# Kernel tuning notes

Measured on AMD Instinct MI355X. Metric: run time of the kernel, lower is better.

Reference implementation:

```python
import jax, jax.numpy as jnp
import numpy as np

N, H = 8192, 1024

def setup_inputs() -> dict:
    key = jax.random.key(0)
    ks = jax.random.split(key, 7)
    s = 1.0 / np.sqrt(H)
    return {
        "x": jax.random.normal(ks[0], (N, H), dtype=jnp.float32),
        "Wq": jax.random.uniform(ks[1], (H, H), dtype=jnp.float32, minval=-s, maxval=s),
        "bq": jax.random.uniform(ks[2], (H,), dtype=jnp.float32, minval=-s, maxval=s),
        "Wk": jax.random.uniform(ks[3], (H, H), dtype=jnp.float32, minval=-s, maxval=s),
        "bk": jax.random.uniform(ks[4], (H,), dtype=jnp.float32, minval=-s, maxval=s),
        "Wv": jax.random.uniform(ks[5], (H, H), dtype=jnp.float32, minval=-s, maxval=s),
        "bv": jax.random.uniform(ks[6], (H,), dtype=jnp.float32, minval=-s, maxval=s),
    }

def reference(x, Wq, bq, Wk, bk, Wv, bv):
    # q/k/v projections: [N, H]
    q = x @ Wq + bq
    k = x @ Wk + bk
    v = x @ Wv + bv
    # full scores [N, N]; NOTE: original has no 1/sqrt(d) scaling
    scores = q @ k.T
    alpha = jax.nn.softmax(scores, axis=1)
    return alpha @ v
```

## Files before the change

### kernel.cpp

```cpp
#include <hip/hip_runtime.h>
#include <hip/hip_bf16.h>
#include <hip/hip_fp16.h>


typedef _Float16 f16x8 __attribute__((ext_vector_type(8)));
typedef float floatx4 __attribute__((ext_vector_type(4)));

__device__ __forceinline__ unsigned short f2h(float f) {
  __half h = __float2half(f);
  return __builtin_bit_cast(unsigned short, h);
}
__device__ __forceinline__ float h2f(unsigned short u) {
  return __half2float(__builtin_bit_cast(__half, u));
}

__device__ __forceinline__ void async16(const void* g, void* l) {
  __builtin_amdgcn_global_load_lds(
      (__attribute__((address_space(1))) unsigned int*)(g),
      (__attribute__((address_space(3))) unsigned int*)(l),
      16, 0, 0);
}


__global__ __launch_bounds__(256) void conv_f32_f16(const float* __restrict__ in,
                                                    unsigned short* __restrict__ out,
                                                    long n) {
  long i = ((long)blockIdx.x * 256 + threadIdx.x) * 4;
  if (i + 3 < n) {
    float4 f = *(const float4*)(in + i);
    ushort4 o;
    o.x = f2h(f.x); o.y = f2h(f.y); o.z = f2h(f.z); o.w = f2h(f.w);
    *(ushort4*)(out + i) = o;
  }
}

__global__ __launch_bounds__(256) void transpose_f32_f16_3(const float* __restrict__ in0,
                                                           const float* __restrict__ in1,
                                                           const float* __restrict__ in2,
                                                           unsigned short* __restrict__ out,
                                                           int rows, int cols) {
  const float* in = (blockIdx.z == 0) ? in0 : (blockIdx.z == 1) ? in1 : in2;
  unsigned short* o = out + (size_t)blockIdx.z * rows * cols;
  __shared__ float tile[32][33];
  int bx = blockIdx.x * 32;
  int by = blockIdx.y * 32;
  int tx = threadIdx.x & 31, ty = threadIdx.x >> 5;
  #pragma unroll
  for (int yy = ty; yy < 32; yy += 8)
    tile[yy][tx] = in[(size_t)(by + yy) * cols + bx + tx];
  __syncthreads();
  #pragma unroll
  for (int yy = ty; yy < 32; yy += 8)
    o[(size_t)(bx + yy) * rows + by + tx] = f2h(tile[tx][yy]);
}

template <int MODE>
__global__ __launch_bounds__(256, 4)
void gemm_bt(const unsigned short* __restrict__ A,
             const unsigned short* __restrict__ B,
             int M, int Nn, int K,
             const float* __restrict__ b0, const float* __restrict__ b1,
             const float* __restrict__ b2,
             unsigned short* __restrict__ out) {
  if constexpr (MODE == 0) {
    B   += (size_t)blockIdx.z * Nn * K;
    out += (size_t)blockIdx.z * M * Nn;
  }
  const float* bias = (MODE != 0) ? nullptr
                      : (blockIdx.z == 0) ? b0 : (blockIdx.z == 1) ? b1 : b2;
  __shared__ unsigned short As[128 * 32];
  __shared__ unsigned short Bs[128 * 32];
  const int tid  = threadIdx.x;
  const int wave = tid >> 6;
  const int lane = tid & 63;
  const int wm = wave >> 1, wn = wave & 1;
  const int quad = lane >> 4, l16 = lane & 15;
  const long bm = (long)blockIdx.y * 128;
  const long bn = (long)blockIdx.x * 128;

  floatx4 acc[4][4] = {};

  const int srow = wave * 32 + (lane >> 2);
  const int scol = (lane & 3) * 8;
  const unsigned short* gA0 = A + (bm + srow) * (long)K + scol;
  const unsigned short* gA1 = gA0 + 16L * K;
  const unsigned short* gB0 = B + (bn + srow) * (long)K + scol;
  const unsigned short* gB1 = gB0 + 16L * K;
  unsigned short* lA0 = &As[(wave * 32) * 32];
  unsigned short* lA1 = &As[(wave * 32 + 16) * 32];
  unsigned short* lB0 = &Bs[(wave * 32) * 32];
  unsigned short* lB1 = &Bs[(wave * 32 + 16) * 32];

  for (int kk = 0; kk < K; kk += 32) {
    async16(gA0 + kk, lA0);
    async16(gA1 + kk, lA1);
    async16(gB0 + kk, lB0);
    async16(gB1 + kk, lB1);
    __syncthreads();
    f16x8 af[4], bfv[4];
    #pragma unroll
    for (int i = 0; i < 4; ++i) {
      af[i]  = *reinterpret_cast<const f16x8*>(&As[(wm * 64 + i * 16 + l16) * 32 + quad * 8]);
      bfv[i] = *reinterpret_cast<const f16x8*>(&Bs[(wn * 64 + i * 16 + l16) * 32 + quad * 8]);
    }
    #pragma unroll
    for (int i = 0; i < 4; ++i)
      #pragma unroll
      for (int j = 0; j < 4; ++j)
        acc[i][j] = __builtin_amdgcn_mfma_f32_16x16x32_f16(af[i], bfv[j], acc[i][j], 0, 0, 0);
    __syncthreads();
  }

  #pragma unroll
  for (int i = 0; i < 4; ++i) {
    const long row0 = bm + wm * 64 + i * 16 + quad * 4;
    #pragma unroll
    for (int j = 0; j < 4; ++j) {
      const long col = bn + wn * 64 + j * 16 + l16;
      const float cb = (MODE == 0) ? bias[col] : 0.0f;
      #pragma unroll
      for (int r = 0; r < 4; ++r)
        out[(row0 + r) * (long)Nn + col] = f2h(acc[i][j][r] + cb);
    }
  }
}

__global__ __launch_bounds__(256) void softmax_compact(unsigned short* __restrict__ S,
                                                       int* __restrict__ nnz, int n) {
  const int row = blockIdx.x;
  const int tid = threadIdx.x;
  const int lane = tid & 63, w = tid >> 6;
  unsigned short* prow = S + (size_t)row * n;
  const __half* hrow = (const __half*)prow;

  float v[32];
  float m = -1e30f;
  #pragma unroll
  for (int i = 0; i < 32; ++i) {
    v[i] = __half2float(hrow[i * 256 + tid]);
    m = fmaxf(m, v[i]);
  }
  #pragma unroll
  for (int off = 32; off > 0; off >>= 1) m = fmaxf(m, __shfl_down(m, off, 64));
  __shared__ float redm[4];
  __shared__ int cnt;
  if (lane == 0) redm[w] = m;
  if (tid == 0) cnt = 0;
  __syncthreads();
  m = fmaxf(fmaxf(redm[0], redm[1]), fmaxf(redm[2], redm[3]));

  float s = 0.0f;
  #pragma unroll
  for (int i = 0; i < 32; ++i) {
    v[i] = __expf(v[i] - m);
    s += v[i];
  }
  #pragma unroll
  for (int off = 32; off > 0; off >>= 1) s += __shfl_down(s, off, 64);
  __shared__ float reds[4];
  if (lane == 0) reds[w] = s;
  __syncthreads();
  s = reds[0] + reds[1] + reds[2] + reds[3];
  const float inv = 1.0f / s;

  unsigned int* pairs = (unsigned int*)prow;
  const int cap = n / 2;
  #pragma unroll
  for (int i = 0; i < 32; ++i) {
    unsigned short h = f2h(v[i] * inv);
    if (h) {
      int p = atomicAdd(&cnt, 1);
      if (p < cap) pairs[p] = ((unsigned int)(i * 256 + tid) << 16) | h;
    }
  }
  __syncthreads();
  if (tid == 0) nnz[row] = (cnt < cap) ? cnt : cap;
}

__global__ __launch_bounds__(256) void pv_sparse(const unsigned short* __restrict__ S,
                                                 const int* __restrict__ nnz,
                                                 const unsigned short* __restrict__ v,
                                                 float* __restrict__ out,
                                                 int n, int h) {
  const int row = blockIdx.x;
  const int tid = threadIdx.x;
  const unsigned int* pairs = (const unsigned int*)(S + (size_t)row * n);
  const int cnt = nnz[row];

  float a0 = 0.f, a1 = 0.f, a2 = 0.f, a3 = 0.f;
  __shared__ unsigned int buf[256];

  for (int base = 0; base < cnt; base += 256) {
    const int mm = min(cnt - base, 256);
    if (tid < mm) buf[tid] = pairs[base + tid];
    __syncthreads();
    int j = 0;
    for (; j + 4 <= mm; j += 4) {
      unsigned int p0 = buf[j], p1 = buf[j + 1], p2 = buf[j + 2], p3 = buf[j + 3];
      ushort4 v0 = *(const ushort4*)(v + (size_t)(p0 >> 16) * h + tid * 4);
      ushort4 v1 = *(const ushort4*)(v + (size_t)(p1 >> 16) * h + tid * 4);
      ushort4 v2 = *(const ushort4*)(v + (size_t)(p2 >> 16) * h + tid * 4);
      ushort4 v3 = *(const ushort4*)(v + (size_t)(p3 >> 16) * h + tid * 4);
      float w0 = h2f(p0 & 0xffff), w1 = h2f(p1 & 0xffff);
      float w2 = h2f(p2 & 0xffff), w3 = h2f(p3 & 0xffff);
      a0 += w0 * h2f(v0.x); a1 += w0 * h2f(v0.y); a2 += w0 * h2f(v0.z); a3 += w0 * h2f(v0.w);
      a0 += w1 * h2f(v1.x); a1 += w1 * h2f(v1.y); a2 += w1 * h2f(v1.z); a3 += w1 * h2f(v1.w);
      a0 += w2 * h2f(v2.x); a1 += w2 * h2f(v2.y); a2 += w2 * h2f(v2.z); a3 += w2 * h2f(v2.w);
      a0 += w3 * h2f(v3.x); a1 += w3 * h2f(v3.y); a2 += w3 * h2f(v3.z); a3 += w3 * h2f(v3.w);
    }
    for (; j < mm; ++j) {
      unsigned int p0 = buf[j];
      ushort4 v0 = *(const ushort4*)(v + (size_t)(p0 >> 16) * h + tid * 4);
      float w0 = h2f(p0 & 0xffff);
      a0 += w0 * h2f(v0.x); a1 += w0 * h2f(v0.y); a2 += w0 * h2f(v0.z); a3 += w0 * h2f(v0.w);
    }
    __syncthreads();
  }
  float4 o = {a0, a1, a2, a3};
  *(float4*)(out + (size_t)row * h + tid * 4) = o;
}

extern "C" void kernel_launch(void* const* d_in, const int* in_sizes, int n_in,
                              void* d_out, int out_size, void* d_ws, size_t ws_size,
                              hipStream_t stream) {
  const int N = 8192, H = 1024;
  const float* x  = (const float*)d_in[0];
  const float* Wq = (const float*)d_in[1];
  const float* bq = (const float*)d_in[2];
  const float* Wk = (const float*)d_in[3];
  const float* bk = (const float*)d_in[4];
  const float* Wv = (const float*)d_in[5];
  const float* bv = (const float*)d_in[6];

  char* p = (char*)d_ws;
  unsigned short* xh  = (unsigned short*)p; p += (size_t)N * H * 2;
  unsigned short* WT  = (unsigned short*)p; p += (size_t)3 * H * H * 2;
  unsigned short* qkv = (unsigned short*)p; p += (size_t)3 * N * H * 2;
  unsigned short* S   = (unsigned short*)p; p += (size_t)N * N * 2;
  int*            nnz = (int*)p;            p += (size_t)N * 4;
  if ((size_t)(p - (char*)d_ws) > ws_size) return;
  unsigned short* qh = qkv;
  unsigned short* kh = qkv + (size_t)N * H;
  unsigned short* vh = qkv + (size_t)2 * N * H;

  conv_f32_f16<<<(N * H / 4 + 255) / 256, 256, 0, stream>>>(x, xh, (long)N * H);
  transpose_f32_f16_3<<<dim3(H / 32, H / 32, 3), 256, 0, stream>>>(Wq, Wk, Wv, WT, H, H);

  gemm_bt<0><<<dim3(H / 128, N / 128, 3), 256, 0, stream>>>(xh, WT, N, H, H,
                                                            bq, bk, bv, qkv);

  gemm_bt<1><<<dim3(N / 128, N / 128), 256, 0, stream>>>(qh, kh, N, N, H,
                                                         nullptr, nullptr, nullptr, S);
  softmax_compact<<<N, 256, 0, stream>>>(S, nnz, N);
  pv_sparse<<<N, 256, 0, stream>>>(S, nnz, vh, (float*)d_out, N, H);
}
```

Measured before the change: 616.0 us.

## Slice sparse PV kernel by column blocks with per-wave row loops

```diff
diff --git a/kernel.cpp b/kernel.cpp
--- a/kernel.cpp
+++ b/kernel.cpp
@@ -5,6 +5,7 @@
 
 typedef _Float16 f16x8 __attribute__((ext_vector_type(8)));
 typedef float floatx4 __attribute__((ext_vector_type(4)));
+typedef float floatx2 __attribute__((ext_vector_type(2)));
 
 __device__ __forceinline__ unsigned short f2h(float f) {
   __half h = __float2half(f);
@@ -167,57 +168,55 @@
   const int cap = n / 2;
   #pragma unroll
   for (int i = 0; i < 32; ++i) {
-    unsigned short h = f2h(v[i] * inv);
-    if (h) {
+    unsigned short hh = f2h(v[i] * inv);
+    if (hh) {
       int p = atomicAdd(&cnt, 1);
-      if (p < cap) pairs[p] = ((unsigned int)(i * 256 + tid) << 16) | h;
+      if (p < cap) pairs[p] = ((unsigned int)(i * 256 + tid) << 16) | hh;
     }
   }
   __syncthreads();
   if (tid == 0) nnz[row] = (cnt < cap) ? cnt : cap;
 }
 
-__global__ __launch_bounds__(256) void pv_sparse(const unsigned short* __restrict__ S,
+__global__ __launch_bounds__(256) void pv_sliced(const unsigned short* __restrict__ S,
                                                  const int* __restrict__ nnz,
                                                  const unsigned short* __restrict__ v,
                                                  float* __restrict__ out,
                                                  int n, int h) {
-  const int row = blockIdx.x;
-  const int tid = threadIdx.x;
-  const unsigned int* pairs = (const unsigned int*)(S + (size_t)row * n);
-  const int cnt = nnz[row];
-
-  float a0 = 0.f, a1 = 0.f, a2 = 0.f, a3 = 0.f;
-  __shared__ unsigned int buf[256];
-
-  for (int base = 0; base < cnt; base += 256) {
-    const int mm = min(cnt - base, 256);
-    if (tid < mm) buf[tid] = pairs[base + tid];
-    __syncthreads();
+  const int wave = threadIdx.x >> 6;
+  const int lane = threadIdx.x & 63;
+  const int colbase = blockIdx.x * 128 + lane * 2;
+  const int row0 = blockIdx.y * 64 + wave * 16;
+  const unsigned short* vs = v + colbase;
+
+  for (int r = 0; r < 16; ++r) {
+    const int row = row0 + r;
+    const unsigned int* pairs = (const unsigned int*)(S + (size_t)row * n);
+    const int cnt = nnz[row];
+    float a0 = 0.f, a1 = 0.f;
     int j = 0;
-    for (; j + 4 <= mm; j += 4) {
-      unsigned int p0 = buf[j], p1 = buf[j + 1], p2 = buf[j + 2], p3 = buf[j + 3];
-      ushort4 v0 = *(const ushort4*)(v + (size_t)(p0 >> 16) * h + tid * 4);
-      ushort4 v1 = *(const ushort4*)(v + (size_t)(p1 >> 16) * h + tid * 4);
-      ushort4 v2 = *(const ushort4*)(v + (size_t)(p2 >> 16) * h + tid * 4);
-      ushort4 v3 = *(const ushort4*)(v + (size_t)(p3 >> 16) * h + tid * 4);
-      float w0 = h2f(p0 & 0xffff), w1 = h2f(p1 & 0xffff);
-      float w2 = h2f(p2 & 0xffff), w3 = h2f(p3 & 0xffff);
-      a0 += w0 * h2f(v0.x); a1 += w0 * h2f(v0.y); a2 += w0 * h2f(v0.z); a3 += w0 * h2f(v0.w);
-      a0 += w1 * h2f(v1.x); a1 += w1 * h2f(v1.y); a2 += w1 * h2f(v1.z); a3 += w1 * h2f(v1.w);
-      a0 += w2 * h2f(v2.x); a1 += w2 * h2f(v2.y); a2 += w2 * h2f(v2.z); a3 += w2 * h2f(v2.w);
-      a0 += w3 * h2f(v3.x); a1 += w3 * h2f(v3.y); a2 += w3 * h2f(v3.z); a3 += w3 * h2f(v3.w);
-    }
-    for (; j < mm; ++j) {
-      unsigned int p0 = buf[j];
-      ushort4 v0 = *(const ushort4*)(v + (size_t)(p0 >> 16) * h + tid * 4);
-      float w0 = h2f(p0 & 0xffff);
-      a0 += w0 * h2f(v0.x); a1 += w0 * h2f(v0.y); a2 += w0 * h2f(v0.z); a3 += w0 * h2f(v0.w);
-    }
-    __syncthreads();
-  }
-  float4 o = {a0, a1, a2, a3};
-  *(float4*)(out + (size_t)row * h + tid * 4) = o;
+    for (; j + 8 <= cnt; j += 8) {
+      unsigned int p[8];
+      #pragma unroll
+      for (int u = 0; u < 8; ++u) p[u] = pairs[j + u];
+      #pragma unroll
+      for (int u = 0; u < 8; ++u) {
+        ushort2 vv = *(const ushort2*)(vs + (size_t)(p[u] >> 16) * h);
+        const float w = h2f(p[u] & 0xffff);
+        a0 += w * h2f(vv.x);
+        a1 += w * h2f(vv.y);
+      }
+    }
+    for (; j < cnt; ++j) {
+      unsigned int p0 = pairs[j];
+      ushort2 vv = *(const ushort2*)(vs + (size_t)(p0 >> 16) * h);
+      const float w = h2f(p0 & 0xffff);
+      a0 += w * h2f(vv.x);
+      a1 += w * h2f(vv.y);
+    }
+    floatx2 o = {a0, a1};
+    __builtin_nontemporal_store(o, (floatx2*)(out + (size_t)row * h + colbase));
+  }
 }
 
 extern "C" void kernel_launch(void* const* d_in, const int* in_sizes, int n_in,
@@ -252,5 +251,5 @@
   gemm_bt<1><<<dim3(N / 128, N / 128), 256, 0, stream>>>(qh, kh, N, N, H,
                                                          nullptr, nullptr, nullptr, S);
   softmax_compact<<<N, 256, 0, stream>>>(S, nnz, N);
-  pv_sparse<<<N, 256, 0, stream>>>(S, nnz, vh, (float*)d_out, N, H);
-}
+  pv_sliced<<<dim3(8, N / 64), 256, 0, stream>>>(S, nnz, vh, (float*)d_out, N, H);
+}
```

After: 652.9 us. 6.0% more time.
